# Kernel optimization log

Hardware: AMD Instinct MI355X
Metric: run time of the kernel (lower is better)

## Reference

```python
import jax, jax.numpy as jnp
import numpy as np

B, N, DIM = 2, 128, 128
H, DH = 8, 32
DI = H * DH          # dim_inner = 256
DM = 2 * DI          # mlp_expansion_factor * dim_inner = 512
MAXDEG = 2
S = 1 + MAXDEG + MAXDEG  # 5
M1, M2 = 3, 5        # 2l+1 for degrees 1,2


def setup_inputs() -> dict:
    key = jax.random.key(0)
    ks = jax.random.split(key, 24)
    rn = lambda k, shp, sc=1.0: jax.random.normal(k, shp, jnp.float32) * sc
    s_d = DIM ** -0.5
    s_m = DM ** -0.5
    s_i = DI ** -0.5
    return {
        "h":    rn(ks[0], (B, N, DIM)),
        "t_ij": rn(ks[1], (B, N, N, DIM)),
        "r1":   rn(ks[2], (B, N, N, M1)),
        "r2":   rn(ks[3], (B, N, N, M2)),
        "x1":   rn(ks[4], (B, N, DIM, M1)),
        "x2":   rn(ks[5], (B, N, DIM, M2)),
        # LayerNorm gains (bias=False)
        "g_hi": jnp.ones((DIM,), jnp.float32),
        "g_hj": jnp.ones((DIM,), jnp.float32),
        # projections (stored as [in, out])
        "Wq":  rn(ks[6],  (DIM, DI), s_d),
        "Wk":  rn(ks[7],  (DIM, DI), s_d),
        "Wv1": rn(ks[8],  (DIM, DM), s_d), "bv1": jnp.zeros((DM,), jnp.float32),
        "Wv2": rn(ks[9],  (DM, S * DI), s_m), "bv2": jnp.zeros((S * DI,), jnp.float32),
        "Wpv1": rn(ks[10], (DIM, DM), s_d), "bpv1": jnp.zeros((DM,), jnp.float32),
        "Wpv2": rn(ks[11], (DM, S * DI), s_m), "bpv2": jnp.zeros((S * DI,), jnp.float32),
        "Wek": rn(ks[12], (DIM, S * DI), s_d),
        "Wev": rn(ks[13], (DIM, S * DI), s_d),
        "Wg":  rn(ks[14], (DIM, H * S), s_d), "bg": jnp.zeros((H * S,), jnp.float32),
        "Wo":  rn(ks[15], (DI, DIM), s_i),
    }


def _ln(x, g):
    mu = x.mean(-1, keepdims=True)
    var = ((x - mu) ** 2).mean(-1, keepdims=True)
    return (x - mu) / jnp.sqrt(var + 1e-5) * g


def reference(h, t_ij, r1, r2, x1, x2, g_hi, g_hj, Wq, Wk, Wv1, bv1, Wv2, bv2,
              Wpv1, bpv1, Wpv2, bpv2, Wek, Wev, Wg, bg, Wo):
    silu = jax.nn.silu
    hi = _ln(h, g_hi)  # b n d
    hj = _ln(h, g_hj)
    # queries/keys: b h n dh
    q = (hi @ Wq).reshape(B, N, H, DH).transpose(0, 2, 1, 3)
    k = (hj @ Wk).reshape(B, N, H, DH).transpose(0, 2, 1, 3)
    # node values / post-attn values: b h n s dh
    v  = (silu(hj @ Wv1 + bv1) @ Wv2 + bv2).reshape(B, N, S, H, DH).transpose(0, 3, 1, 2, 4)
    pv = (silu(hj @ Wpv1 + bpv1) @ Wpv2 + bpv2).reshape(B, N, S, H, DH).transpose(0, 3, 1, 2, 4)
    # edge keys/values: b h i j s dh
    ek = silu(t_ij @ Wek).reshape(B, N, N, S, H, DH).transpose(0, 4, 1, 2, 3, 5)
    ev = (t_ij @ Wev).reshape(B, N, N, S, H, DH).transpose(0, 4, 1, 2, 3, 5)
    # keys elementwise-conditioned by edge keys, then score over dh
    sim = jnp.einsum('bhid,bhjd,bhijsd->bhijs', q, k, ek)
    attn = jax.nn.softmax(sim, axis=3)  # softmax over j (dim=-2 of b h i j s)
    # sea_ij: b h i j s dh
    sea = attn[..., None] * v[:, :, None] + ev * pv[:, :, None]
    # gates: b h i 1 s 1
    gates = jax.nn.sigmoid(hi @ Wg + bg).reshape(B, N, H, S).transpose(0, 2, 1, 3)
    out = sea * gates[:, :, :, None, :, None]
    # merge heads -> b i j s (h dh), combine -> b i j s dim
    out = out.transpose(0, 2, 3, 4, 1, 5).reshape(B, N, N, S, DI) @ Wo
    # split along s: (1, maxdeg, maxdeg) = (h_scales, r_scales, x_scales)
    h_out = h + out[..., 0, :].sum(axis=2)  # sum over j
    x1_out = (jnp.einsum('bjdm,bijd->bidm', x1, out[..., 3, :])
              + jnp.einsum('bijm,bijd->bidm', r1, out[..., 1, :]))
    x2_out = (jnp.einsum('bjdm,bijd->bidm', x2, out[..., 4, :])
              + jnp.einsum('bijm,bijd->bidm', r2, out[..., 2, :]))
    return (h_out, x1_out, x2_out)
```

## Files before the change

kernel.cpp:

```cpp
#include <hip/hip_runtime.h>
#include <math.h>

#define BB 2
#define NN 128
#define DD 128
#define DI 256
#define DM 512
#define SS 5
#define SDI 1280
#define HS 40
#define M1 3
#define M2 5

typedef __attribute__((ext_vector_type(8))) short bf16x8_t;
typedef __attribute__((ext_vector_type(4))) float f32x4_t;
typedef __attribute__((ext_vector_type(4))) float f32x4v;

#define MFMA __builtin_amdgcn_mfma_f32_16x16x32_bf16

__device__ __forceinline__ float sigm(float x){ return __fdividef(1.0f, 1.0f + __expf(-x)); }
__device__ __forceinline__ unsigned short f2bf(float f){
    union { float f; unsigned u; } v; v.f = f;
    unsigned r = v.u + 0x7FFFu + ((v.u>>16)&1u);
    return (unsigned short)(r>>16);
}
__device__ __forceinline__ unsigned pk2(float a, float b){
    return (unsigned)f2bf(a) | ((unsigned)f2bf(b)<<16);
}
__device__ __forceinline__ float bflo(unsigned u){ union{unsigned u; float f;} v; v.u = u<<16; return v.f; }
__device__ __forceinline__ float bfhi(unsigned u){ union{unsigned u; float f;} v; v.u = u & 0xFFFF0000u; return v.f; }

__global__ __launch_bounds__(256) void prep(
    const float* __restrict__ h,
    const float* __restrict__ g_hi, const float* __restrict__ g_hj,
    const float* __restrict__ Wq, const float* __restrict__ Wk,
    const float* __restrict__ Wv1, const float* __restrict__ Wpv1,
    const float* __restrict__ Wg,
    const float* __restrict__ Wek, const float* __restrict__ Wev,
    const float* __restrict__ Wo, const float* __restrict__ Wv2,
    const float* __restrict__ Wpv2,
    const float* __restrict__ x1, const float* __restrict__ x2,
    unsigned short* __restrict__ hi_ws, unsigned short* __restrict__ hj_ws,
    unsigned short* __restrict__ WekT, unsigned short* __restrict__ WevT,
    unsigned short* __restrict__ WoT, unsigned short* __restrict__ W2T,
    unsigned short* __restrict__ WnT,
    float* __restrict__ x1T, float* __restrict__ x2T)
{
    const int bx = blockIdx.x, tid = threadIdx.x;
    __shared__ unsigned short sLT[64*65];
    if (bx < 408){
        const float* src; unsigned short* dst; int W, ldD, R0, C0;
        int t = bx;
        if (t < 160){ src=Wv2;  dst=W2T;            W=SDI; ldD=DM;  R0=(t%20)*64; C0=(t/20)*64; }
        else if (t < 320){ t-=160; src=Wpv2; dst=W2T + SDI*DM; W=SDI; ldD=DM; R0=(t%20)*64; C0=(t/20)*64; }
        else if (t < 360){ t-=320; src=Wek; dst=WekT; W=SDI; ldD=DD; R0=(t%20)*64; C0=(t/20)*64; }
        else if (t < 400){ t-=360; src=Wev; dst=WevT; W=SDI; ldD=DD; R0=(t%20)*64; C0=(t/20)*64; }
        else { t-=400; src=Wo; dst=WoT; W=DD; ldD=DI; R0=(t%2)*64; C0=(t/2)*64; }
        const int tx = tid & 63, ty = tid >> 6;
        #pragma unroll
        for (int k=0;k<16;++k){
            int c = C0 + 4*k + ty;
            sLT[tx*65 + 4*k + ty] = f2bf(src[(size_t)c*W + R0 + tx]);
        }
        __syncthreads();
        #pragma unroll
        for (int k=0;k<16;++k){
            int rr = 4*k + ty;
            dst[(size_t)(R0+rr)*ldD + C0 + tx] = sLT[rr*65 + tx];
        }
    } else if (bx < 664){
        const int node = bx - 408;
        if (tid < 64){
            float h0 = h[node*DD + tid], h1 = h[node*DD + 64 + tid];
            float s1 = h0 + h1, s2 = h0*h0 + h1*h1;
            #pragma unroll
            for (int off=32; off; off>>=1){ s1 += __shfl_xor(s1,off); s2 += __shfl_xor(s2,off); }
            float mu   = s1*(1.0f/DD);
            float var  = s2*(1.0f/DD) - mu*mu;
            float rstd = rsqrtf(var + 1e-5f);
            float c0 = (h0-mu)*rstd, c1 = (h1-mu)*rstd;
            hi_ws[node*DD + tid]      = f2bf(c0*g_hi[tid]);
            hi_ws[node*DD + 64 + tid] = f2bf(c1*g_hi[64+tid]);
            hj_ws[node*DD + tid]      = f2bf(c0*g_hj[tid]);
            hj_ws[node*DD + 64 + tid] = f2bf(c1*g_hj[64+tid]);
        }
        for (int f = node*256 + tid; f < 1584*DD; f += 256*256){
            int row = f >> 7, d = f & 127;
            float v;
            if (row < 256)       v = Wq[d*DI + row];
            else if (row < 304){ int c = row-256; v = (c < HS) ? Wg[d*HS + c] : 0.0f; }
            else if (row < 560)  v = Wk[d*DI + (row-304)];
            else if (row < 1072) v = Wv1[d*DM + (row-560)];
            else                 v = Wpv1[d*DM + (row-1072)];
            WnT[f] = f2bf(v);
        }
    } else {
        const int t = bx - 664;
        const int bb = t >> 7, j = t & 127;
        const int d = tid & 127, half = tid >> 7;
        if (half == 0){
            #pragma unroll
            for (int m=0;m<M1;++m)
                x1T[((size_t)(bb*M1+m)*NN + j)*DD + d] =
                    x1[(((size_t)bb*NN + j)*DD + d)*M1 + m];
        } else {
            #pragma unroll
            for (int m=0;m<M2;++m)
                x2T[((size_t)(bb*M2+m)*NN + j)*DD + d] =
                    x2[(((size_t)bb*NN + j)*DD + d)*M2 + m];
        }
    }
}

__global__ __launch_bounds__(256,4) void node_gemm(
    const unsigned short* __restrict__ WnT,
    const unsigned short* __restrict__ hi_ws, const unsigned short* __restrict__ hj_ws,
    const float* __restrict__ bg, const float* __restrict__ bv1, const float* __restrict__ bpv1,
    float* __restrict__ q_ws, float* __restrict__ k_ws,
    float* __restrict__ g_ws, unsigned short* __restrict__ hid_ws)
{
    const int bx = blockIdx.x;
    const int tile = bx % 99, nq = bx / 99;
    const int tid = threadIdx.x, lane = tid&63, w = tid>>6;
    const int l15 = lane&15, g4 = lane>>4;
    const int ntile = nq*4 + w;
    const unsigned short* A  = WnT + (size_t)(tile*16 + l15)*DD + 8*g4;
    const unsigned short* Bp = ((tile < 19) ? hi_ws : hj_ws) + (size_t)(ntile*16 + l15)*DD + 8*g4;
    f32x4_t c = {0.f,0.f,0.f,0.f};
    #pragma unroll
    for (int ks=0; ks<4; ++ks)
        c = MFMA(*(const bf16x8_t*)(A + 32*ks), *(const bf16x8_t*)(Bp + 32*ks), c, 0,0,0);
    const int node = ntile*16 + l15;
    const int col0 = tile*16 + 4*g4;
    if (tile < 16){
        f32x4_t* dst = (f32x4_t*)(q_ws + (size_t)node*DI + col0);
        *dst = c;
    } else if (tile < 19){
        #pragma unroll
        for (int r=0;r<4;++r){
            int cc = col0 + r - 256;
            if (cc < HS) g_ws[node*HS + cc] = sigm(c[r] + bg[cc]);
        }
    } else if (tile < 35){
        f32x4_t* dst = (f32x4_t*)(k_ws + (size_t)node*DI + (col0-304));
        *dst = c;
    } else if (tile < 67){
        int cc = col0 - 560;
        float s0 = c[0]+bv1[cc], s1 = c[1]+bv1[cc+1], s2 = c[2]+bv1[cc+2], s3 = c[3]+bv1[cc+3];
        s0 *= sigm(s0); s1 *= sigm(s1); s2 *= sigm(s2); s3 *= sigm(s3);
        uint2 pkk; pkk.x = pk2(s0,s1); pkk.y = pk2(s2,s3);
        *(uint2*)(hid_ws + (size_t)node*1024 + cc) = pkk;
    } else {
        int cc = col0 - 1072;
        float s0 = c[0]+bpv1[cc], s1 = c[1]+bpv1[cc+1], s2 = c[2]+bpv1[cc+2], s3 = c[3]+bpv1[cc+3];
        s0 *= sigm(s0); s1 *= sigm(s1); s2 *= sigm(s2); s3 *= sigm(s3);
        uint2 pkk; pkk.x = pk2(s0,s1); pkk.y = pk2(s2,s3);
        *(uint2*)(hid_ws + (size_t)node*1024 + 512 + cc) = pkk;
    }
}

__global__ __launch_bounds__(256,4) void v2_gemm(
    const unsigned short* __restrict__ W2T,
    const unsigned short* __restrict__ hid_ws,
    const float* __restrict__ bv2, const float* __restrict__ bpv2,
    unsigned short* __restrict__ vpv_ws)
{
    const int bx = blockIdx.x;
    const int otile = bx % 160, nq = bx / 160;
    const int tid = threadIdx.x, lane = tid&63, w = tid>>6;
    const int l15 = lane&15, g4 = lane>>4;
    const int ntile = nq*4 + w;
    const int obase = otile*16;
    const int koff = (obase < SDI) ? 0 : 512;
    const unsigned short* A  = W2T + (size_t)(obase + l15)*DM + 8*g4;
    const unsigned short* Bp = hid_ws + (size_t)(ntile*16 + l15)*1024 + koff + 8*g4;
    f32x4_t c = {0.f,0.f,0.f,0.f};
    #pragma unroll
    for (int ks=0; ks<16; ++ks)
        c = MFMA(*(const bf16x8_t*)(A + 32*ks), *(const bf16x8_t*)(Bp + 32*ks), c, 0,0,0);
    const int node = ntile*16 + l15;
    const int o0 = obase + 4*g4;
    const float* bias = (obase < SDI) ? bv2 : bpv2;
    const int ob = (obase < SDI) ? o0 : (o0 - SDI);
    float v0 = c[0]+bias[ob], v1 = c[1]+bias[ob+1], v2 = c[2]+bias[ob+2], v3 = c[3]+bias[ob+3];
    uint2 pkk; pkk.x = pk2(v0,v1); pkk.y = pk2(v2,v3);
    *(uint2*)(vpv_ws + (size_t)node*2560 + o0) = pkk;
}

#define SH_T   0
#define SH_QK  16384
#define SH_SIM 49152
#define SH_Q   59392

__global__ __launch_bounds__(512,4) void simh(
    const float* __restrict__ t_ij,
    const unsigned short* __restrict__ WekT,
    const float* __restrict__ q_ws, const float* __restrict__ k_ws,
    float* __restrict__ sim_ws)
{
    __shared__ __align__(16) char sm[60416];
    float* sSIM = (float*)(sm + SH_SIM);
    float* sQf  = (float*)(sm + SH_Q);

    const int bx0 = blockIdx.x;
    const int bx = ((bx0 & 7) << 6) | (bx0 >> 3);
    const int node = bx >> 1, jh = bx & 1;
    const int b = node >> 7;
    const int j0 = jh*64;
    const int tid = threadIdx.x, lane = tid&63, w = tid>>6;
    const int l15 = lane&15, g4 = lane>>4;

    if (tid < DI) sQf[tid] = q_ws[(size_t)node*DI + tid];
    {
        const int j = tid>>3, seg = tid&7;
        const float* src = t_ij + (size_t)(node*NN + j0 + j)*DD + seg*16;
        char* row = sm + SH_T + j*256;
        const int swz = (j&7)<<4;
        #pragma unroll
        for (int u=0;u<4;++u){
            f32x4v tv = __builtin_nontemporal_load((const f32x4v*)(src + 4*u));
            uint2 pkk; pkk.x = pk2(tv[0],tv[1]); pkk.y = pk2(tv[2],tv[3]);
            *(uint2*)(row + ((2*(seg*16+4*u)) ^ swz)) = pkk;
        }
    }
    __syncthreads();
    {
        const int j = tid>>3, seg = tid&7;
        const float* kr = k_ws + (size_t)(b*NN + j0 + j)*DI + seg*32;
        char* row = sm + SH_QK + j*512;
        const int swz = (j&7)<<4;
        #pragma unroll
        for (int u=0;u<8;++u){
            float4 kv = *(const float4*)(kr + 4*u);
            const float* qv = sQf + seg*32 + 4*u;
            uint2 pkk; pkk.x = pk2(kv.x*qv[0], kv.y*qv[1]); pkk.y = pk2(kv.z*qv[2], kv.w*qv[3]);
            *(uint2*)(row + ((2*(seg*32+4*u)) ^ swz)) = pkk;
        }
    }
    bf16x8_t bT[4][4];
    #pragma unroll
    for (int jt=0;jt<4;++jt){
        const int jc = jt*16 + l15;
        const char* row = sm + SH_T + jc*256;
        const int swz = (jc&7)<<4;
        #pragma unroll
        for (int ks=0;ks<4;++ks)
            bT[jt][ks] = *(const bf16x8_t*)(row + ((2*(32*ks+8*g4)) ^ swz));
    }
    __syncthreads();

    for (int p5=0; p5<5; ++p5){
        const int p = w + 8*p5;
        const unsigned short* ap = WekT + (size_t)(2*p)*16*DD + (size_t)l15*DD + 8*g4;
        bf16x8_t a0[4], a1[4];
        #pragma unroll
        for (int ks=0;ks<4;++ks){
            a0[ks] = *(const bf16x8_t*)(ap + 32*ks);
            a1[ks] = *(const bf16x8_t*)(ap + 16*DD + 32*ks);
        }
        const int hs = w*SS + p5;
        const int o0 = 32*p + 4*g4;
        const int qk0 = o0 & 255;
        #pragma unroll
        for (int jt=0;jt<4;++jt){
            f32x4_t c0 = {0.f,0.f,0.f,0.f}, c1 = {0.f,0.f,0.f,0.f};
            #pragma unroll
            for (int ks=0;ks<4;++ks){
                c0 = MFMA(a0[ks], bT[jt][ks], c0, 0,0,0);
                c1 = MFMA(a1[ks], bT[jt][ks], c1, 0,0,0);
            }
            const int jr = jt*16 + l15;
            const char* qrow = sm + SH_QK + jr*512;
            const int swz = (jr&7)<<4;
            uint2 u0 = *(const uint2*)(qrow + ((2*qk0) ^ swz));
            uint2 u1 = *(const uint2*)(qrow + ((2*(qk0+16)) ^ swz));
            float part =
                (c0[0]*sigm(c0[0]))*bflo(u0.x) + (c0[1]*sigm(c0[1]))*bfhi(u0.x)
              + (c0[2]*sigm(c0[2]))*bflo(u0.y) + (c0[3]*sigm(c0[3]))*bfhi(u0.y)
              + (c1[0]*sigm(c1[0]))*bflo(u1.x) + (c1[1]*sigm(c1[1]))*bfhi(u1.x)
              + (c1[2]*sigm(c1[2]))*bflo(u1.y) + (c1[3]*sigm(c1[3]))*bfhi(u1.y);
            part += __shfl_xor(part, 16);
            part += __shfl_xor(part, 32);
            if (g4 == 0) sSIM[jr*HS + hs] = part;
        }
    }
    __syncthreads();
    {
        float* dst = sim_ws + (size_t)node*NN*HS + j0*HS;
        for (int t2=tid; t2<64*HS; t2+=512) dst[t2] = sSIM[t2];
    }
}

__global__ __launch_bounds__(256) void softmax_k(
    float* __restrict__ sim_ws, const float* __restrict__ g_ws)
{
    const int node = blockIdx.x;
    const int tid = threadIdx.x, lane = tid&63, w = tid>>6;
    float* srow = sim_ws + (size_t)node*NN*HS;
    #pragma unroll
    for (int u=0; u<10; ++u){
        const int hs = w*10 + u;
        const float gt = g_ws[node*HS + hs];
        float v0 = srow[lane*HS + hs];
        float v1 = srow[(lane+64)*HS + hs];
        float m = fmaxf(v0,v1);
        #pragma unroll
        for (int off=32; off; off>>=1) m = fmaxf(m, __shfl_xor(m,off));
        float e0 = __expf(v0-m), e1 = __expf(v1-m);
        float ssum = e0+e1;
        #pragma unroll
        for (int off=32; off; off>>=1) ssum += __shfl_xor(ssum,off);
        float inv = __fdividef(gt, ssum);
        srow[lane*HS + hs]      = e0*inv;
        srow[(lane+64)*HS + hs] = e1*inv;
    }
}

#define OH_T   0
#define OH_P   16384
#define OH_AT  49152
#define OH_G   59392
#define OH_W1  59552
#define OH_W2  60320

#define EV_BODY(S, EPILOG)                                                        \
    _Pragma("unroll")                                                             \
    for (int mloc=0; mloc<2; ++mloc){                                             \
        const int mt = w*2 + mloc;                                                \
        const int m0 = mt*16 + 4*g4;                                              \
        uint2 vvr[4], ppr[4];                                                     \
        _Pragma("unroll")                                                         \
        for (int jt=0;jt<4;++jt){                                                 \
            const unsigned short* vb = vpv_ws + (size_t)(b*NN + j0 + jt*16 + l15)*2560 + (S)*DI + m0; \
            vvr[jt] = *(const uint2*)vb;                                          \
            ppr[jt] = *(const uint2*)(vb + SDI);                                  \
        }                                                                         \
        const unsigned short* ap = WevT + (size_t)((S)*DI + mt*16 + l15)*DD + 8*g4; \
        bf16x8_t aa[4];                                                           \
        _Pragma("unroll")                                                         \
        for (int ks=0;ks<4;++ks) aa[ks] = *(const bf16x8_t*)(ap + 32*ks);         \
        const int hh = mt >> 1;                                                   \
        const float gtv = sG[hh*SS + (S)];                                        \
        _Pragma("unroll")                                                         \
        for (int jt=0;jt<4;++jt){                                                 \
            const int jc = jt*16 + l15;                                           \
            bf16x8_t bT[4];                                                       \
            {   const char* row_ = sm + OH_T + jc*256;                            \
                const int swz_ = (jc&7)<<4;                                       \
                _Pragma("unroll")                                                 \
                for (int ks=0;ks<4;++ks)                                          \
                    bT[ks] = *(const bf16x8_t*)(row_ + ((2*(32*ks+8*g4)) ^ swz_)); } \
            f32x4_t c = {0.f,0.f,0.f,0.f};                                        \
            _Pragma("unroll")                                                     \
            for (int ks=0;ks<4;++ks) c = MFMA(aa[ks], bT[ks], c, 0,0,0);          \
            const float atv = sATT[jc*HS + hh*SS + (S)];                          \
            float g_[4];                                                          \
            g_[0] = atv*bflo(vvr[jt].x) + gtv*c[0]*bflo(ppr[jt].x);               \
            g_[1] = atv*bfhi(vvr[jt].x) + gtv*c[1]*bfhi(ppr[jt].x);               \
            g_[2] = atv*bflo(vvr[jt].y) + gtv*c[2]*bflo(ppr[jt].y);               \
            g_[3] = atv*bfhi(vvr[jt].y) + gtv*c[3]*bfhi(ppr[jt].y);               \
            EPILOG                                                                \
        }                                                                         \
    }

#define WO_X(XT, MM, AX)                                                          \
    _Pragma("unroll")                                                             \
    for (int jt=0; jt<4; ++jt){                                                   \
        float xv[4*(MM)];                                                         \
        _Pragma("unroll")                                                         \
        for (int r_=0;r_<4;++r_){                                                 \
            const int jr = j0 + jt*16 + 4*g4 + r_;                                \
            _Pragma("unroll")                                                     \
            for (int m_=0;m_<(MM);++m_)                                           \
                xv[r_*(MM)+m_] = XT[((size_t)(b*(MM)+m_)*NN + jr)*DD + d];        \
        }                                                                         \
        const int arow = jt*16 + l15;                                             \
        const char* pbp = sm + OH_P + arow*512;                                   \
        const int aswz = (arow&7)<<4;                                             \
        f32x4_t c = {0.f,0.f,0.f,0.f};                                            \
        _Pragma("unroll")                                                         \
        for (int ks=0;ks<8;++ks){                                                 \
            bf16x8_t a = *(const bf16x8_t*)(pbp + ((64*ks + 16*g4) ^ aswz));      \
            c = MFMA(a, bWo[ks], c, 0,0,0);                                       \
        }                                                                         \
        _Pragma("unroll")                                                         \
        for (int r_=0;r_<4;++r_){                                                 \
            _Pragma("unroll")                                                     \
            for (int m_=0;m_<(MM);++m_) AX[m_] = fmaf(xv[r_*(MM)+m_], c[r_], AX[m_]); \
        }                                                                         \
    }

#define RED_WRITE(VAL, ROW, T_)                                                   \
    { float v_ = (VAL);                                                           \
      v_ += __shfl_xor(v_,1); v_ += __shfl_xor(v_,2);                             \
      v_ += __shfl_xor(v_,4); v_ += __shfl_xor(v_,8);                             \
      if (l15 == 0)                                                               \
          pdst[(ROW)*256 + (w*2 + ((T_)>>2))*16 + 4*g4 + ((T_)&3)] = v_; }

__global__ __launch_bounds__(512,4) void outh(
    const float* __restrict__ t_ij,
    const unsigned short* __restrict__ WevT, const unsigned short* __restrict__ WoT,
    const unsigned short* __restrict__ vpv_ws,
    const float* __restrict__ attn_ws,
    const float* __restrict__ g_ws,
    const float* __restrict__ r1, const float* __restrict__ r2,
    const float* __restrict__ x1T, const float* __restrict__ x2T,
    float* __restrict__ p012, float* __restrict__ p34)
{
    __shared__ __align__(16) char sm[61600];
    float* sATT = (float*)(sm + OH_AT);
    float* sG   = (float*)(sm + OH_G);
    float* sW1  = (float*)(sm + OH_W1);
    float* sW2  = (float*)(sm + OH_W2);

    const int bx0 = blockIdx.x;
    const int bx = ((bx0 & 7) << 6) | (bx0 >> 3);
    const int node = bx >> 1, jh = bx & 1;
    const int b = node >> 7;
    const int j0 = jh*64;
    const int tid = threadIdx.x, lane = tid&63, w = tid>>6;
    const int l15 = lane&15, g4 = lane>>4;

    {
        const int j = tid>>3, seg = tid&7;
        const float* src = t_ij + (size_t)(node*NN + j0 + j)*DD + seg*16;
        char* row = sm + OH_T + j*256;
        const int swz = (j&7)<<4;
        #pragma unroll
        for (int u=0;u<4;++u){
            f32x4v tv = __builtin_nontemporal_load((const f32x4v*)(src + 4*u));
            uint2 pkk; pkk.x = pk2(tv[0],tv[1]); pkk.y = pk2(tv[2],tv[3]);
            *(uint2*)(row + ((2*(seg*16+4*u)) ^ swz)) = pkk;
        }
    }
    {
        const float* asrc = attn_ws + (size_t)node*NN*HS + j0*HS;
        for (int t2=tid; t2<64*HS; t2+=512) sATT[t2] = asrc[t2];
    }
    if (tid < HS) sG[tid] = g_ws[node*HS + tid];
    if (tid < 64*M1) sW1[tid] = r1[((size_t)node*NN + j0)*M1 + tid];
    if (tid < 64*M2) sW2[tid] = r2[((size_t)node*NN + j0)*M2 + tid];
    __syncthreads();

    float* pdst = p012 + (size_t)(jh*256 + node)*9*256;

    {
        float a0[8] = {0,0,0,0,0,0,0,0};
        EV_BODY(0, {
            _Pragma("unroll")
            for (int k_=0;k_<4;++k_) a0[mloc*4+k_] += g_[k_];
        })
        #pragma unroll
        for (int t_=0;t_<8;++t_) RED_WRITE(a0[t_], 0, t_)
    }
    {
        float a1[M1][8];
        #pragma unroll
        for (int m_=0;m_<M1;++m_)
            #pragma unroll
            for (int t_=0;t_<8;++t_) a1[m_][t_] = 0.f;
        EV_BODY(1, {
            _Pragma("unroll")
            for (int m_=0;m_<M1;++m_){
                const float wgt = sW1[jc*M1 + m_];
                _Pragma("unroll")
                for (int k_=0;k_<4;++k_) a1[m_][mloc*4+k_] = fmaf(wgt, g_[k_], a1[m_][mloc*4+k_]);
            }
        })
        #pragma unroll
        for (int m_=0;m_<M1;++m_)
            #pragma unroll
            for (int t_=0;t_<8;++t_) RED_WRITE(a1[m_][t_], 1+m_, t_)
    }
    {
        float a2[M2][8];
        #pragma unroll
        for (int m_=0;m_<M2;++m_)
            #pragma unroll
            for (int t_=0;t_<8;++t_) a2[m_][t_] = 0.f;
        EV_BODY(2, {
            _Pragma("unroll")
            for (int m_=0;m_<M2;++m_){
                const float wgt = sW2[jc*M2 + m_];
                _Pragma("unroll")
                for (int k_=0;k_<4;++k_) a2[m_][mloc*4+k_] = fmaf(wgt, g_[k_], a2[m_][mloc*4+k_]);
            }
        })
        #pragma unroll
        for (int m_=0;m_<M2;++m_)
            #pragma unroll
            for (int t_=0;t_<8;++t_) RED_WRITE(a2[m_][t_], 4+m_, t_)
    }

    const int d = w*16 + l15;
    bf16x8_t bWo[8];
    {
        const unsigned short* wr = WoT + (size_t)d*DI + 8*g4;
        #pragma unroll
        for (int ks=0;ks<8;++ks) bWo[ks] = *(const bf16x8_t*)(wr + 32*ks);
    }
    float ax1[M1] = {0.f,0.f,0.f};
    float ax2[M2] = {0.f,0.f,0.f,0.f,0.f};

    EV_BODY(3, {
        uint2 pkk; pkk.x = pk2(g_[0],g_[1]); pkk.y = pk2(g_[2],g_[3]);
        *(uint2*)(sm + OH_P + jc*512 + ((2*m0) ^ ((jc&7)<<4))) = pkk;
    })
    __syncthreads();
    WO_X(x1T, M1, ax1)
    __syncthreads();
    EV_BODY(4, {
        uint2 pkk; pkk.x = pk2(g_[0],g_[1]); pkk.y = pk2(g_[2],g_[3]);
        *(uint2*)(sm + OH_P + jc*512 + ((2*m0) ^ ((jc&7)<<4))) = pkk;
    })
    __syncthreads();
    WO_X(x2T, M2, ax2)

    {
        float v0 = ax1[0], v1 = ax1[1], v2 = ax1[2];
        float v3 = ax2[0], v4 = ax2[1], v5 = ax2[2], v6 = ax2[3], v7 = ax2[4];
        v0 += __shfl_xor(v0,16); v0 += __shfl_xor(v0,32);
        v1 += __shfl_xor(v1,16); v1 += __shfl_xor(v1,32);
        v2 += __shfl_xor(v2,16); v2 += __shfl_xor(v2,32);
        v3 += __shfl_xor(v3,16); v3 += __shfl_xor(v3,32);
        v4 += __shfl_xor(v4,16); v4 += __shfl_xor(v4,32);
        v5 += __shfl_xor(v5,16); v5 += __shfl_xor(v5,32);
        v6 += __shfl_xor(v6,16); v6 += __shfl_xor(v6,32);
        v7 += __shfl_xor(v7,16); v7 += __shfl_xor(v7,32);
        if (g4 == 0){
            float* pb = p34 + (size_t)bx*8*DD + d;
            pb[0*DD] = v0; pb[1*DD] = v1; pb[2*DD] = v2;
            pb[3*DD] = v3; pb[4*DD] = v4; pb[5*DD] = v5;
            pb[6*DD] = v6; pb[7*DD] = v7;
        }
    }
}

__global__ __launch_bounds__(128) void combine(
    const float* __restrict__ h, const unsigned short* __restrict__ WoT,
    const float* __restrict__ p012, const float* __restrict__ p34,
    float* __restrict__ out_h, float* __restrict__ out_x1, float* __restrict__ out_x2)
{
    __shared__ float sZ[256*12];
    const int node = blockIdx.x, d = threadIdx.x;
    const float* pa = p012 + ((size_t)node*9)*256;
    const float* pb = p012 + ((size_t)(256 + node)*9)*256;
    for (int t=d; t<2304; t+=128){
        int m = t >> 8, c = t & 255;
        sZ[c*12 + m] = pa[t] + pb[t];
    }
    __syncthreads();
    float az[9] = {0.f,0.f,0.f,0.f,0.f,0.f,0.f,0.f,0.f};
    const unsigned short* wr = WoT + (size_t)d*DI;
    for (int cb=0; cb<32; ++cb){
        uint4 wv = *(const uint4*)(wr + cb*8);
        float wk[8];
        wk[0]=bflo(wv.x); wk[1]=bfhi(wv.x); wk[2]=bflo(wv.y); wk[3]=bfhi(wv.y);
        wk[4]=bflo(wv.z); wk[5]=bfhi(wv.z); wk[6]=bflo(wv.w); wk[7]=bfhi(wv.w);
        #pragma unroll
        for (int k=0;k<8;++k){
            const float* zb = sZ + (cb*8+k)*12;
            float4 za = *(const float4*)zb;
            float4 zbv = *(const float4*)(zb+4);
            float z8 = zb[8];
            az[0] = fmaf(za.x,  wk[k], az[0]);
            az[1] = fmaf(za.y,  wk[k], az[1]);
            az[2] = fmaf(za.z,  wk[k], az[2]);
            az[3] = fmaf(za.w,  wk[k], az[3]);
            az[4] = fmaf(zbv.x, wk[k], az[4]);
            az[5] = fmaf(zbv.y, wk[k], az[5]);
            az[6] = fmaf(zbv.z, wk[k], az[6]);
            az[7] = fmaf(zbv.w, wk[k], az[7]);
            az[8] = fmaf(z8,    wk[k], az[8]);
        }
    }
    float p34v[8];
    #pragma unroll
    for (int row=0; row<8; ++row){
        p34v[row] = p34[((size_t)(node*2+0)*8 + row)*DD + d]
                  + p34[((size_t)(node*2+1)*8 + row)*DD + d];
    }
    out_h[(size_t)node*DD + d] = h[(size_t)node*DD + d] + az[0];
    #pragma unroll
    for (int m=0;m<M1;++m)
        out_x1[((size_t)node*DD + d)*M1 + m] = az[1+m] + p34v[m];
    #pragma unroll
    for (int m=0;m<M2;++m)
        out_x2[((size_t)node*DD + d)*M2 + m] = az[4+m] + p34v[3+m];
}

extern "C" void kernel_launch(void* const* d_in, const int* in_sizes, int n_in,
                              void* d_out, int out_size, void* d_ws, size_t ws_size,
                              hipStream_t stream)
{
    (void)in_sizes; (void)n_in; (void)out_size; (void)ws_size;
    const float* h    = (const float*)d_in[0];
    const float* t_ij = (const float*)d_in[1];
    const float* r1   = (const float*)d_in[2];
    const float* r2   = (const float*)d_in[3];
    const float* x1   = (const float*)d_in[4];
    const float* x2   = (const float*)d_in[5];
    const float* g_hi = (const float*)d_in[6];
    const float* g_hj = (const float*)d_in[7];
    const float* Wq   = (const float*)d_in[8];
    const float* Wk   = (const float*)d_in[9];
    const float* Wv1  = (const float*)d_in[10];
    const float* bv1  = (const float*)d_in[11];
    const float* Wv2  = (const float*)d_in[12];
    const float* bv2  = (const float*)d_in[13];
    const float* Wpv1 = (const float*)d_in[14];
    const float* bpv1 = (const float*)d_in[15];
    const float* Wpv2 = (const float*)d_in[16];
    const float* bpv2 = (const float*)d_in[17];
    const float* Wek  = (const float*)d_in[18];
    const float* Wev  = (const float*)d_in[19];
    const float* Wg   = (const float*)d_in[20];
    const float* bg   = (const float*)d_in[21];
    const float* Wo   = (const float*)d_in[22];

    float* fb     = (float*)d_ws;
    float* q_ws   = fb;
    float* k_ws   = q_ws   + 65536;
    float* g_ws   = k_ws   + 65536;
    float* sim_ws = g_ws   + 10240;
    float* p012   = sim_ws + 1310720;
    float* p34    = p012   + 1179648;
    float* x1T    = p34    + 524288;
    float* x2T    = x1T    + 98304;
    unsigned short* hi_ws  = (unsigned short*)(x2T + 163840);
    unsigned short* hj_ws  = hi_ws  + 32768;
    unsigned short* hid_ws = hj_ws  + 32768;
    unsigned short* vpv_ws = hid_ws + 262144;
    unsigned short* WekT   = vpv_ws + 655360;
    unsigned short* WevT   = WekT   + 163840;
    unsigned short* WoT    = WevT   + 163840;
    unsigned short* W2T    = WoT    + 32768;
    unsigned short* WnT    = W2T    + 1310720;

    float* out_h  = (float*)d_out;
    float* out_x1 = out_h  + BB*NN*DD;
    float* out_x2 = out_x1 + BB*NN*DD*M1;

    prep<<<920, 256, 0, stream>>>(h, g_hi, g_hj, Wq, Wk, Wv1, Wpv1, Wg,
        Wek, Wev, Wo, Wv2, Wpv2, x1, x2,
        hi_ws, hj_ws, WekT, WevT, WoT, W2T, WnT, x1T, x2T);

    node_gemm<<<396, 256, 0, stream>>>(WnT, hi_ws, hj_ws, bg, bv1, bpv1,
        q_ws, k_ws, g_ws, hid_ws);

    v2_gemm<<<640, 256, 0, stream>>>(W2T, hid_ws, bv2, bpv2, vpv_ws);

    simh<<<512, 512, 0, stream>>>(t_ij, WekT, q_ws, k_ws, sim_ws);

    softmax_k<<<256, 256, 0, stream>>>(sim_ws, g_ws);

    outh<<<512, 512, 0, stream>>>(t_ij, WevT, WoT, vpv_ws, sim_ws, g_ws,
        r1, r2, x1T, x2T, p012, p34);

    combine<<<256, 128, 0, stream>>>(h, WoT, p012, p34, out_h, out_x1, out_x2);
}
```

Measured before the change: 172.5 us.

## Shrink LDS and register footprint in simh/outh to raise occupancy

In simh, the sim staging buffer in shared memory is removed so partial scores go straight to global memory, and the B fragments are loaded per tile instead of held for all tiles, cutting registers. In outh, the P tile buffer is halved by splitting the Wo contraction into two K-halves with extra barriers, and the EV loop is unrolled explicitly. Both kernels raise launch bounds to 6 blocks/CU. The cost is more LDS reads in simh, scattered global stores, and four extra __syncthreads in outh.

Result: slower. 419.4 us (+143.0%).

```diff
diff --git a/kernel.cpp b/kernel.cpp
--- a/kernel.cpp
+++ b/kernel.cpp
@@ -189,17 +189,15 @@
 
 #define SH_T   0
 #define SH_QK  16384
-#define SH_SIM 49152
-#define SH_Q   59392
-
-__global__ __launch_bounds__(512,4) void simh(
+#define SH_Q   49152
+
+__global__ __launch_bounds__(512,6) void simh(
     const float* __restrict__ t_ij,
     const unsigned short* __restrict__ WekT,
     const float* __restrict__ q_ws, const float* __restrict__ k_ws,
     float* __restrict__ sim_ws)
 {
-    __shared__ __align__(16) char sm[60416];
-    float* sSIM = (float*)(sm + SH_SIM);
+    __shared__ __align__(16) char sm[50176];
     float* sQf  = (float*)(sm + SH_Q);
 
     const int bx0 = blockIdx.x;
@@ -237,18 +235,9 @@
             *(uint2*)(row + ((2*(seg*32+4*u)) ^ swz)) = pkk;
         }
     }
-    bf16x8_t bT[4][4];
-    #pragma unroll
-    for (int jt=0;jt<4;++jt){
-        const int jc = jt*16 + l15;
-        const char* row = sm + SH_T + jc*256;
-        const int swz = (jc&7)<<4;
-        #pragma unroll
-        for (int ks=0;ks<4;++ks)
-            bT[jt][ks] = *(const bf16x8_t*)(row + ((2*(32*ks+8*g4)) ^ swz));
-    }
-    __syncthreads();
-
+    __syncthreads();
+
+    float* srow_out = sim_ws + (size_t)node*NN*HS + j0*HS;
     for (int p5=0; p5<5; ++p5){
         const int p = w + 8*p5;
         const unsigned short* ap = WekT + (size_t)(2*p)*16*DD + (size_t)l15*DD + 8*g4;
@@ -263,13 +252,21 @@
         const int qk0 = o0 & 255;
         #pragma unroll
         for (int jt=0;jt<4;++jt){
+            const int jr = jt*16 + l15;
+            bf16x8_t bT[4];
+            {
+                const char* row = sm + SH_T + jr*256;
+                const int swz = (jr&7)<<4;
+                #pragma unroll
+                for (int ks=0;ks<4;++ks)
+                    bT[ks] = *(const bf16x8_t*)(row + ((2*(32*ks+8*g4)) ^ swz));
+            }
             f32x4_t c0 = {0.f,0.f,0.f,0.f}, c1 = {0.f,0.f,0.f,0.f};
             #pragma unroll
             for (int ks=0;ks<4;++ks){
-                c0 = MFMA(a0[ks], bT[jt][ks], c0, 0,0,0);
-                c1 = MFMA(a1[ks], bT[jt][ks], c1, 0,0,0);
+                c0 = MFMA(a0[ks], bT[ks], c0, 0,0,0);
+                c1 = MFMA(a1[ks], bT[ks], c1, 0,0,0);
             }
-            const int jr = jt*16 + l15;
             const char* qrow = sm + SH_QK + jr*512;
             const int swz = (jr&7)<<4;
             uint2 u0 = *(const uint2*)(qrow + ((2*qk0) ^ swz));
@@ -281,13 +278,8 @@
               + (c1[2]*sigm(c1[2]))*bflo(u1.y) + (c1[3]*sigm(c1[3]))*bfhi(u1.y);
             part += __shfl_xor(part, 16);
             part += __shfl_xor(part, 32);
-            if (g4 == 0) sSIM[jr*HS + hs] = part;
-        }
-    }
-    __syncthreads();
-    {
-        float* dst = sim_ws + (size_t)node*NN*HS + j0*HS;
-        for (int t2=tid; t2<64*HS; t2+=512) dst[t2] = sSIM[t2];
+            if (g4 == 0) srow_out[jr*HS + hs] = part;
+        }
     }
 }
 
@@ -318,15 +310,14 @@
 
 #define OH_T   0
 #define OH_P   16384
-#define OH_AT  49152
-#define OH_G   59392
-#define OH_W1  59552
-#define OH_W2  60320
-
-#define EV_BODY(S, EPILOG)                                                        \
-    _Pragma("unroll")                                                             \
-    for (int mloc=0; mloc<2; ++mloc){                                             \
-        const int mt = w*2 + mloc;                                                \
+#define OH_AT  32768
+#define OH_G   43008
+#define OH_W1  43168
+#define OH_W2  43936
+
+#define EV_ONE(S, MT, EPILOG)                                                     \
+    {                                                                             \
+        const int mt = (MT);                                                      \
         const int m0 = mt*16 + 4*g4;                                              \
         uint2 vvr[4], ppr[4];                                                     \
         _Pragma("unroll")                                                         \
@@ -363,7 +354,11 @@
         }                                                                         \
     }
 
-#define WO_X(XT, MM, AX)                                                          \
+#define P_WRITE                                                                   \
+    { uint2 pkk; pkk.x = pk2(g_[0],g_[1]); pkk.y = pk2(g_[2],g_[3]);              \
+      *(uint2*)(sm + OH_P + jc*256 + ((2*(m0 & 127)) ^ ((jc&7)<<4))) = pkk; }
+
+#define WO_XH(XT, MM, AX, H)                                                      \
     _Pragma("unroll")                                                             \
     for (int jt=0; jt<4; ++jt){                                                   \
         float xv[4*(MM)];                                                         \
@@ -375,13 +370,13 @@
                 xv[r_*(MM)+m_] = XT[((size_t)(b*(MM)+m_)*NN + jr)*DD + d];        \
         }                                                                         \
         const int arow = jt*16 + l15;                                             \
-        const char* pbp = sm + OH_P + arow*512;                                   \
+        const char* pbp = sm + OH_P + arow*256;                                   \
         const int aswz = (arow&7)<<4;                                             \
         f32x4_t c = {0.f,0.f,0.f,0.f};                                            \
         _Pragma("unroll")                                                         \
-        for (int ks=0;ks<8;++ks){                                                 \
+        for (int ks=0;ks<4;++ks){                                                 \
             bf16x8_t a = *(const bf16x8_t*)(pbp + ((64*ks + 16*g4) ^ aswz));      \
-            c = MFMA(a, bWo[ks], c, 0,0,0);                                       \
+            c = MFMA(a, bWo[4*(H)+ks], c, 0,0,0);                                 \
         }                                                                         \
         _Pragma("unroll")                                                         \
         for (int r_=0;r_<4;++r_){                                                 \
@@ -397,7 +392,7 @@
       if (l15 == 0)                                                               \
           pdst[(ROW)*256 + (w*2 + ((T_)>>2))*16 + 4*g4 + ((T_)&3)] = v_; }
 
-__global__ __launch_bounds__(512,4) void outh(
+__global__ __launch_bounds__(512,6) void outh(
     const float* __restrict__ t_ij,
     const unsigned short* __restrict__ WevT, const unsigned short* __restrict__ WoT,
     const unsigned short* __restrict__ vpv_ws,
@@ -407,7 +402,7 @@
     const float* __restrict__ x1T, const float* __restrict__ x2T,
     float* __restrict__ p012, float* __restrict__ p34)
 {
-    __shared__ __align__(16) char sm[61600];
+    __shared__ __align__(16) char sm[45216];
     float* sATT = (float*)(sm + OH_AT);
     float* sG   = (float*)(sm + OH_G);
     float* sW1  = (float*)(sm + OH_W1);
@@ -446,10 +441,14 @@
 
     {
         float a0[8] = {0,0,0,0,0,0,0,0};
-        EV_BODY(0, {
+        EV_ONE(0, 2*w, {
             _Pragma("unroll")
-            for (int k_=0;k_<4;++k_) a0[mloc*4+k_] += g_[k_];
+            for (int k_=0;k_<4;++k_) a0[k_] += g_[k_];
         })
+        EV_ONE(0, 2*w+1, {
+            _Pragma("unroll")
+            for (int k_=0;k_<4;++k_) a0[4+k_] += g_[k_];
+        })
         #pragma unroll
         for (int t_=0;t_<8;++t_) RED_WRITE(a0[t_], 0, t_)
     }
@@ -459,14 +458,22 @@
         for (int m_=0;m_<M1;++m_)
             #pragma unroll
             for (int t_=0;t_<8;++t_) a1[m_][t_] = 0.f;
-        EV_BODY(1, {
+        EV_ONE(1, 2*w, {
             _Pragma("unroll")
             for (int m_=0;m_<M1;++m_){
                 const float wgt = sW1[jc*M1 + m_];
                 _Pragma("unroll")
-                for (int k_=0;k_<4;++k_) a1[m_][mloc*4+k_] = fmaf(wgt, g_[k_], a1[m_][mloc*4+k_]);
+                for (int k_=0;k_<4;++k_) a1[m_][k_] = fmaf(wgt, g_[k_], a1[m_][k_]);
             }
         })
+        EV_ONE(1, 2*w+1, {
+            _Pragma("unroll")
+            for (int m_=0;m_<M1;++m_){
+                const float wgt = sW1[jc*M1 + m_];
+                _Pragma("unroll")
+                for (int k_=0;k_<4;++k_) a1[m_][4+k_] = fmaf(wgt, g_[k_], a1[m_][4+k_]);
+            }
+        })
         #pragma unroll
         for (int m_=0;m_<M1;++m_)
             #pragma unroll
@@ -478,14 +485,22 @@
         for (int m_=0;m_<M2;++m_)
             #pragma unroll
             for (int t_=0;t_<8;++t_) a2[m_][t_] = 0.f;
-        EV_BODY(2, {
+        EV_ONE(2, 2*w, {
             _Pragma("unroll")
             for (int m_=0;m_<M2;++m_){
                 const float wgt = sW2[jc*M2 + m_];
                 _Pragma("unroll")
-                for (int k_=0;k_<4;++k_) a2[m_][mloc*4+k_] = fmaf(wgt, g_[k_], a2[m_][mloc*4+k_]);
+                for (int k_=0;k_<4;++k_) a2[m_][k_] = fmaf(wgt, g_[k_], a2[m_][k_]);
             }
         })
+        EV_ONE(2, 2*w+1, {
+            _Pragma("unroll")
+            for (int m_=0;m_<M2;++m_){
+                const float wgt = sW2[jc*M2 + m_];
+                _Pragma("unroll")
+                for (int k_=0;k_<4;++k_) a2[m_][4+k_] = fmaf(wgt, g_[k_], a2[m_][4+k_]);
+            }
+        })
         #pragma unroll
         for (int m_=0;m_<M2;++m_)
             #pragma unroll
@@ -502,19 +517,21 @@
     float ax1[M1] = {0.f,0.f,0.f};
     float ax2[M2] = {0.f,0.f,0.f,0.f,0.f};
 
-    EV_BODY(3, {
-        uint2 pkk; pkk.x = pk2(g_[0],g_[1]); pkk.y = pk2(g_[2],g_[3]);
-        *(uint2*)(sm + OH_P + jc*512 + ((2*m0) ^ ((jc&7)<<4))) = pkk;
-    })
-    __syncthreads();
-    WO_X(x1T, M1, ax1)
-    __syncthreads();
-    EV_BODY(4, {
-        uint2 pkk; pkk.x = pk2(g_[0],g_[1]); pkk.y = pk2(g_[2],g_[3]);
-        *(uint2*)(sm + OH_P + jc*512 + ((2*m0) ^ ((jc&7)<<4))) = pkk;
-    })
-    __syncthreads();
-    WO_X(x2T, M2, ax2)
+    EV_ONE(3, w, P_WRITE)
+    __syncthreads();
+    WO_XH(x1T, M1, ax1, 0)
+    __syncthreads();
+    EV_ONE(3, 8+w, P_WRITE)
+    __syncthreads();
+    WO_XH(x1T, M1, ax1, 1)
+    __syncthreads();
+    EV_ONE(4, w, P_WRITE)
+    __syncthreads();
+    WO_XH(x2T, M2, ax2, 0)
+    __syncthreads();
+    EV_ONE(4, 8+w, P_WRITE)
+    __syncthreads();
+    WO_XH(x2T, M2, ax2, 1)
 
     {
         float v0 = ax1[0], v1 = ax1[1], v2 = ax1[2];
```

## Split fused output kernel into separate s012 and s34 kernels

Applied to the files above, without the earlier changes.

Splits the monolithic outh kernel into two kernels. out_s012 handles the scale 0-2 reductions and out_s34 handles the scale 3-4 Wo projections against x1/x2. Each kernel holds only the attention slices it needs in shared memory, so the per-block LDS footprint shrinks, especially for the s012 kernel, which should allow more resident blocks. The cost is that t_ij is loaded and converted twice and there is one extra kernel launch.

Result: slower. 182.3 us (+5.7%).

```diff
diff --git a/kernel.cpp b/kernel.cpp
--- a/kernel.cpp
+++ b/kernel.cpp
@@ -316,14 +316,7 @@
     }
 }
 
-#define OH_T   0
-#define OH_P   16384
-#define OH_AT  49152
-#define OH_G   59392
-#define OH_W1  59552
-#define OH_W2  60320
-
-#define EV_BODY(S, EPILOG)                                                        \
+#define EV_BODY(S, ATTIDX, EPILOG)                                                \
     _Pragma("unroll")                                                             \
     for (int mloc=0; mloc<2; ++mloc){                                             \
         const int mt = w*2 + mloc;                                                \
@@ -345,7 +338,7 @@
         for (int jt=0;jt<4;++jt){                                                 \
             const int jc = jt*16 + l15;                                           \
             bf16x8_t bT[4];                                                       \
-            {   const char* row_ = sm + OH_T + jc*256;                            \
+            {   const char* row_ = sm + jc*256;                                   \
                 const int swz_ = (jc&7)<<4;                                       \
                 _Pragma("unroll")                                                 \
                 for (int ks=0;ks<4;++ks)                                          \
@@ -353,7 +346,7 @@
             f32x4_t c = {0.f,0.f,0.f,0.f};                                        \
             _Pragma("unroll")                                                     \
             for (int ks=0;ks<4;++ks) c = MFMA(aa[ks], bT[ks], c, 0,0,0);          \
-            const float atv = sATT[jc*HS + hh*SS + (S)];                          \
+            const float atv = sATT[ATTIDX];                                       \
             float g_[4];                                                          \
             g_[0] = atv*bflo(vvr[jt].x) + gtv*c[0]*bflo(ppr[jt].x);               \
             g_[1] = atv*bfhi(vvr[jt].x) + gtv*c[1]*bfhi(ppr[jt].x);               \
@@ -362,6 +355,117 @@
             EPILOG                                                                \
         }                                                                         \
     }
+
+#define RED_WRITE(VAL, ROW, T_)                                                   \
+    { float v_ = (VAL);                                                           \
+      v_ += __shfl_xor(v_,1); v_ += __shfl_xor(v_,2);                             \
+      v_ += __shfl_xor(v_,4); v_ += __shfl_xor(v_,8);                             \
+      if (l15 == 0)                                                               \
+          pdst[(ROW)*256 + (w*2 + ((T_)>>2))*16 + 4*g4 + ((T_)&3)] = v_; }
+
+__global__ __launch_bounds__(512,4) void out_s012(
+    const float* __restrict__ t_ij,
+    const unsigned short* __restrict__ WevT,
+    const unsigned short* __restrict__ vpv_ws,
+    const float* __restrict__ attn_ws,
+    const float* __restrict__ g_ws,
+    const float* __restrict__ r1, const float* __restrict__ r2,
+    float* __restrict__ p012)
+{
+    __shared__ __align__(16) char sm[24736];
+    float* sATT = (float*)(sm + 16384);
+    float* sG   = (float*)(sm + 22528);
+    float* sW1  = (float*)(sm + 22688);
+    float* sW2  = (float*)(sm + 23456);
+
+    const int bx0 = blockIdx.x;
+    const int bx = ((bx0 & 7) << 6) | (bx0 >> 3);
+    const int node = bx >> 1, jh = bx & 1;
+    const int b = node >> 7;
+    const int j0 = jh*64;
+    const int tid = threadIdx.x, lane = tid&63, w = tid>>6;
+    const int l15 = lane&15, g4 = lane>>4;
+
+    {
+        const int j = tid>>3, seg = tid&7;
+        const float* src = t_ij + (size_t)(node*NN + j0 + j)*DD + seg*16;
+        char* row = sm + j*256;
+        const int swz = (j&7)<<4;
+        #pragma unroll
+        for (int u=0;u<4;++u){
+            f32x4v tv = __builtin_nontemporal_load((const f32x4v*)(src + 4*u));
+            uint2 pkk; pkk.x = pk2(tv[0],tv[1]); pkk.y = pk2(tv[2],tv[3]);
+            *(uint2*)(row + ((2*(seg*16+4*u)) ^ swz)) = pkk;
+        }
+    }
+    {
+        const float* asrc = attn_ws + (size_t)node*NN*HS + j0*HS;
+        for (int t2=tid; t2<64*24; t2+=512){
+            int j = t2/24, rem = t2 - 24*j, hh = rem/3, s = rem - 3*hh;
+            sATT[t2] = asrc[j*HS + hh*SS + s];
+        }
+    }
+    if (tid < HS) sG[tid] = g_ws[node*HS + tid];
+    if (tid < 64*M1) sW1[tid] = r1[((size_t)node*NN + j0)*M1 + tid];
+    if (tid < 64*M2) sW2[tid] = r2[((size_t)node*NN + j0)*M2 + tid];
+    __syncthreads();
+
+    float* pdst = p012 + (size_t)(jh*256 + node)*9*256;
+
+    {
+        float a0[8] = {0,0,0,0,0,0,0,0};
+        EV_BODY(0, jc*24 + hh*3 + 0, {
+            _Pragma("unroll")
+            for (int k_=0;k_<4;++k_) a0[mloc*4+k_] += g_[k_];
+        })
+        #pragma unroll
+        for (int t_=0;t_<8;++t_) RED_WRITE(a0[t_], 0, t_)
+    }
+    {
+        float a1[M1][8];
+        #pragma unroll
+        for (int m_=0;m_<M1;++m_)
+            #pragma unroll
+            for (int t_=0;t_<8;++t_) a1[m_][t_] = 0.f;
+        EV_BODY(1, jc*24 + hh*3 + 1, {
+            _Pragma("unroll")
+            for (int m_=0;m_<M1;++m_){
+                const float wgt = sW1[jc*M1 + m_];
+                _Pragma("unroll")
+                for (int k_=0;k_<4;++k_) a1[m_][mloc*4+k_] = fmaf(wgt, g_[k_], a1[m_][mloc*4+k_]);
+            }
+        })
+        #pragma unroll
+        for (int m_=0;m_<M1;++m_)
+            #pragma unroll
+            for (int t_=0;t_<8;++t_) RED_WRITE(a1[m_][t_], 1+m_, t_)
+    }
+    {
+        float a2[M2][8];
+        #pragma unroll
+        for (int m_=0;m_<M2;++m_)
+            #pragma unroll
+            for (int t_=0;t_<8;++t_) a2[m_][t_] = 0.f;
+        EV_BODY(2, jc*24 + hh*3 + 2, {
+            _Pragma("unroll")
+            for (int m_=0;m_<M2;++m_){
+                const float wgt = sW2[jc*M2 + m_];
+                _Pragma("unroll")
+                for (int k_=0;k_<4;++k_) a2[m_][mloc*4+k_] = fmaf(wgt, g_[k_], a2[m_][mloc*4+k_]);
+            }
+        })
+        #pragma unroll
+        for (int m_=0;m_<M2;++m_)
+            #pragma unroll
+            for (int t_=0;t_<8;++t_) RED_WRITE(a2[m_][t_], 4+m_, t_)
+    }
+}
+
+#define O34_P  16384
+
+#define P_WRITE34                                                                 \
+    { uint2 pkk; pkk.x = pk2(g_[0],g_[1]); pkk.y = pk2(g_[2],g_[3]);              \
+      *(uint2*)(sm + O34_P + jc*512 + ((2*m0) ^ ((jc&7)<<4))) = pkk; }
 
 #define WO_X(XT, MM, AX)                                                          \
     _Pragma("unroll")                                                             \
@@ -375,7 +479,7 @@
                 xv[r_*(MM)+m_] = XT[((size_t)(b*(MM)+m_)*NN + jr)*DD + d];        \
         }                                                                         \
         const int arow = jt*16 + l15;                                             \
-        const char* pbp = sm + OH_P + arow*512;                                   \
+        const char* pbp = sm + O34_P + arow*512;                                  \
         const int aswz = (arow&7)<<4;                                             \
         f32x4_t c = {0.f,0.f,0.f,0.f};                                            \
         _Pragma("unroll")                                                         \
@@ -390,28 +494,18 @@
         }                                                                         \
     }
 
-#define RED_WRITE(VAL, ROW, T_)                                                   \
-    { float v_ = (VAL);                                                           \
-      v_ += __shfl_xor(v_,1); v_ += __shfl_xor(v_,2);                             \
-      v_ += __shfl_xor(v_,4); v_ += __shfl_xor(v_,8);                             \
-      if (l15 == 0)                                                               \
-          pdst[(ROW)*256 + (w*2 + ((T_)>>2))*16 + 4*g4 + ((T_)&3)] = v_; }
-
-__global__ __launch_bounds__(512,4) void outh(
+__global__ __launch_bounds__(512,4) void out_s34(
     const float* __restrict__ t_ij,
     const unsigned short* __restrict__ WevT, const unsigned short* __restrict__ WoT,
     const unsigned short* __restrict__ vpv_ws,
     const float* __restrict__ attn_ws,
     const float* __restrict__ g_ws,
-    const float* __restrict__ r1, const float* __restrict__ r2,
     const float* __restrict__ x1T, const float* __restrict__ x2T,
-    float* __restrict__ p012, float* __restrict__ p34)
-{
-    __shared__ __align__(16) char sm[61600];
-    float* sATT = (float*)(sm + OH_AT);
-    float* sG   = (float*)(sm + OH_G);
-    float* sW1  = (float*)(sm + OH_W1);
-    float* sW2  = (float*)(sm + OH_W2);
+    float* __restrict__ p34)
+{
+    __shared__ __align__(16) char sm[53408];
+    float* sATT = (float*)(sm + 49152);
+    float* sG   = (float*)(sm + 53248);
 
     const int bx0 = blockIdx.x;
     const int bx = ((bx0 & 7) << 6) | (bx0 >> 3);
@@ -424,7 +518,7 @@
     {
         const int j = tid>>3, seg = tid&7;
         const float* src = t_ij + (size_t)(node*NN + j0 + j)*DD + seg*16;
-        char* row = sm + OH_T + j*256;
+        char* row = sm + j*256;
         const int swz = (j&7)<<4;
         #pragma unroll
         for (int u=0;u<4;++u){
@@ -435,84 +529,29 @@
     }
     {
         const float* asrc = attn_ws + (size_t)node*NN*HS + j0*HS;
-        for (int t2=tid; t2<64*HS; t2+=512) sATT[t2] = asrc[t2];
+        for (int t2=tid; t2<64*16; t2+=512){
+            int j = t2>>4, rem = t2 & 15, hh = rem>>1, s = 3 + (rem&1);
+            sATT[t2] = asrc[j*HS + hh*SS + s];
+        }
     }
     if (tid < HS) sG[tid] = g_ws[node*HS + tid];
-    if (tid < 64*M1) sW1[tid] = r1[((size_t)node*NN + j0)*M1 + tid];
-    if (tid < 64*M2) sW2[tid] = r2[((size_t)node*NN + j0)*M2 + tid];
-    __syncthreads();
-
-    float* pdst = p012 + (size_t)(jh*256 + node)*9*256;
-
-    {
-        float a0[8] = {0,0,0,0,0,0,0,0};
-        EV_BODY(0, {
-            _Pragma("unroll")
-            for (int k_=0;k_<4;++k_) a0[mloc*4+k_] += g_[k_];
-        })
-        #pragma unroll
-        for (int t_=0;t_<8;++t_) RED_WRITE(a0[t_], 0, t_)
-    }
-    {
-        float a1[M1][8];
-        #pragma unroll
-        for (int m_=0;m_<M1;++m_)
-            #pragma unroll
-            for (int t_=0;t_<8;++t_) a1[m_][t_] = 0.f;
-        EV_BODY(1, {
-            _Pragma("unroll")
-            for (int m_=0;m_<M1;++m_){
-                const float wgt = sW1[jc*M1 + m_];
-                _Pragma("unroll")
-                for (int k_=0;k_<4;++k_) a1[m_][mloc*4+k_] = fmaf(wgt, g_[k_], a1[m_][mloc*4+k_]);
-            }
-        })
-        #pragma unroll
-        for (int m_=0;m_<M1;++m_)
-            #pragma unroll
-            for (int t_=0;t_<8;++t_) RED_WRITE(a1[m_][t_], 1+m_, t_)
-    }
-    {
-        float a2[M2][8];
-        #pragma unroll
-        for (int m_=0;m_<M2;++m_)
-            #pragma unroll
-            for (int t_=0;t_<8;++t_) a2[m_][t_] = 0.f;
-        EV_BODY(2, {
-            _Pragma("unroll")
-            for (int m_=0;m_<M2;++m_){
-                const float wgt = sW2[jc*M2 + m_];
-                _Pragma("unroll")
-                for (int k_=0;k_<4;++k_) a2[m_][mloc*4+k_] = fmaf(wgt, g_[k_], a2[m_][mloc*4+k_]);
-            }
-        })
-        #pragma unroll
-        for (int m_=0;m_<M2;++m_)
-            #pragma unroll
-            for (int t_=0;t_<8;++t_) RED_WRITE(a2[m_][t_], 4+m_, t_)
-    }
+    bf16x8_t bWo[8];
+    {
+        const unsigned short* wr = WoT + (size_t)(w*16 + l15)*DI + 8*g4;
+        #pragma unroll
+        for (int ks=0;ks<8;++ks) bWo[ks] = *(const bf16x8_t*)(wr + 32*ks);
+    }
+    __syncthreads();
 
     const int d = w*16 + l15;
-    bf16x8_t bWo[8];
-    {
-        const unsigned short* wr = WoT + (size_t)d*DI + 8*g4;
-        #pragma unroll
-        for (int ks=0;ks<8;++ks) bWo[ks] = *(const bf16x8_t*)(wr + 32*ks);
-    }
     float ax1[M1] = {0.f,0.f,0.f};
     float ax2[M2] = {0.f,0.f,0.f,0.f,0.f};
 
-    EV_BODY(3, {
-        uint2 pkk; pkk.x = pk2(g_[0],g_[1]); pkk.y = pk2(g_[2],g_[3]);
-        *(uint2*)(sm + OH_P + jc*512 + ((2*m0) ^ ((jc&7)<<4))) = pkk;
-    })
+    EV_BODY(3, jc*16 + hh*2 + 0, P_WRITE34)
     __syncthreads();
     WO_X(x1T, M1, ax1)
     __syncthreads();
-    EV_BODY(4, {
-        uint2 pkk; pkk.x = pk2(g_[0],g_[1]); pkk.y = pk2(g_[2],g_[3]);
-        *(uint2*)(sm + OH_P + jc*512 + ((2*m0) ^ ((jc&7)<<4))) = pkk;
-    })
+    EV_BODY(4, jc*16 + hh*2 + 1, P_WRITE34)
     __syncthreads();
     WO_X(x2T, M2, ax2)
 
@@ -654,8 +693,11 @@
 
     softmax_k<<<256, 256, 0, stream>>>(sim_ws, g_ws);
 
-    outh<<<512, 512, 0, stream>>>(t_ij, WevT, WoT, vpv_ws, sim_ws, g_ws,
-        r1, r2, x1T, x2T, p012, p34);
+    out_s012<<<512, 512, 0, stream>>>(t_ij, WevT, vpv_ws, sim_ws, g_ws,
+        r1, r2, p012);
+
+    out_s34<<<512, 512, 0, stream>>>(t_ij, WevT, WoT, vpv_ws, sim_ws, g_ws,
+        x1T, x2T, p34);
 
     combine<<<256, 128, 0, stream>>>(h, WoT, p012, p34, out_h, out_x1, out_x2);
 }
```
